# Optimization experiments

Measured on AMD Instinct MI355X. Metric: run time of the kernel, lower is better.

The kernel has to match this reference:

```python
import math
import jax, jax.numpy as jnp
import numpy as np

N = 50000          # nodes
E = 800000         # edges
IN_DIM = 128
HID = 128
OUT_DIM = 64
LAYER_NUM = 8      # -> LAYER_NUM - 2 = 6 GCN2Conv layers
NUM_CONVS = LAYER_NUM - 2
ALPHA = 0.1
THETA = 0.5
# PyG GCN2Conv: beta = log(theta / layer + 1); here every conv was built with layer = layer_num + 1
BETA = math.log(THETA / (LAYER_NUM + 1) + 1.0)


def setup_inputs() -> dict:
    key = jax.random.key(0)
    ks = jax.random.split(key, 10)
    x = jax.random.normal(ks[0], (N, IN_DIM), dtype=jnp.float32)
    edge_src = jax.random.randint(ks[1], (E,), 0, N, dtype=jnp.int32)
    edge_dst = jax.random.randint(ks[2], (E,), 0, N, dtype=jnp.int32)
    edge_weight = jax.random.uniform(ks[3], (E,), dtype=jnp.float32)
    s0 = 1.0 / math.sqrt(IN_DIM)
    s1 = 1.0 / math.sqrt(HID)
    W0 = jax.random.uniform(ks[4], (IN_DIM, HID), dtype=jnp.float32, minval=-s0, maxval=s0)
    b0 = jnp.zeros((HID,), dtype=jnp.float32)
    W1 = jax.random.uniform(ks[5], (HID, OUT_DIM), dtype=jnp.float32, minval=-s1, maxval=s1)
    b1 = jnp.zeros((OUT_DIM,), dtype=jnp.float32)
    conv_ws = jax.random.uniform(ks[6], (NUM_CONVS, HID, HID), dtype=jnp.float32, minval=-s1, maxval=s1)
    return {"x": x, "edge_src": edge_src, "edge_dst": edge_dst, "edge_weight": edge_weight,
            "W0": W0, "b0": b0, "W1": W1, "b1": b1, "conv_ws": conv_ws}


def reference(x, edge_src, edge_dst, edge_weight, W0, b0, W1, b1, conv_ws):
    # linear[0] + relu (dropout=0.0 -> identity)
    h = jnp.maximum(x @ W0 + b0, 0.0)          # [N, HID]
    x0 = h
    for i in range(NUM_CONVS):
        # weighted neighbor sum: out[i] = sum_{(j->i)} w_ji * h[j]
        msgs = h[edge_src] * edge_weight[:, None]               # [E, HID]
        agg = jax.ops.segment_sum(msgs, edge_dst, num_segments=N)
        # GCN2Conv (shared_weights=True): z = (1-alpha)*Ah + alpha*x0; out = (1-beta)*z + beta*(z W)
        z = agg * (1.0 - ALPHA) + ALPHA * x0
        h = z * (1.0 - BETA) + BETA * (z @ conv_ws[i])
        h = jnp.maximum(h, 0.0)
    return h @ W1 + b1                          # [N, OUT_DIM]
```

## Files before the change

kernel.cpp:

```cpp
#include <hip/hip_runtime.h>
#include <cstdint>
#include <cstddef>


#define NN 50000
#define EE 800000

constexpr float ALPHA   = 0.1f;
constexpr float BETA_C  = 0.05406722127027574f;

constexpr int NB = (NN + 255) / 256;
constexpr int HB = (EE + 255) / 256;
constexpr int PREP_TOT = 128 * 128 + 6 * 128 * 128 + 64 * 128;
constexpr int PB = (PREP_TOT + 255) / 256;
constexpr int SLICE = NN / 8;
constexpr int GA = (NN + 63) / 64;
constexpr int AGGB = 8 * ((GA + 1) / 2);

typedef unsigned short u16;
typedef unsigned int   u32;
typedef __attribute__((ext_vector_type(8))) short short8;
typedef __attribute__((ext_vector_type(4))) float f32x4;

__device__ __forceinline__ float bf2f(u16 u) {
    union { float f; u32 i; } c; c.i = ((u32)u) << 16; return c.f;
}
__device__ __forceinline__ u16 f2bf(float f) {
    union { float f; u32 i; } c; c.f = f;
    u32 r = c.i + 0x7fffu + ((c.i >> 16) & 1u);
    return (u16)(r >> 16);
}

__global__ void k_hist_prep(const int* __restrict__ edst, int* __restrict__ deg,
                            const float* __restrict__ W0, const float* __restrict__ cw,
                            const float* __restrict__ W1, u16* __restrict__ w0t,
                            u16* __restrict__ wft, u16* __restrict__ w1t, int E) {
    int b = blockIdx.x;
    if (b < HB) {
        int i = b * 256 + threadIdx.x;
        if (i < E) atomicAdd(&deg[edst[i]], 1);
    } else {
        int i = (b - HB) * 256 + threadIdx.x;
        if (i < 16384) {
            int n = i >> 7, k = i & 127;
            w0t[i] = f2bf(W0[k * 128 + n]);
        } else if (i < 16384 + 6 * 16384) {
            int r = i - 16384;
            int l = r >> 14; int t = r & 16383;
            int n = t >> 7, k = t & 127;
            float v = BETA_C * cw[l * 16384 + k * 128 + n]
                      + ((k == n) ? (1.f - BETA_C) : 0.f);
            wft[r] = f2bf(v);
        } else if (i < PREP_TOT) {
            int r = i - (16384 + 6 * 16384);
            int n = r >> 7, k = r & 127;
            w1t[r] = f2bf(W1[k * 64 + n]);
        }
    }
}

__global__ __launch_bounds__(256) void k_scan_lb(const int* __restrict__ deg,
                                                 int* __restrict__ bsum,
                                                 int* __restrict__ offs,
                                                 int* __restrict__ cur) {
    __shared__ int sh[256];
    __shared__ int sw[4];
    const int c = blockIdx.x, tid = threadIdx.x;
    const int i = c * 256 + tid;
    int v = (i < NN) ? deg[i] : 0;
    sh[tid] = v;
    __syncthreads();
#pragma unroll
    for (int o = 1; o < 256; o <<= 1) {
        int u = (tid >= o) ? sh[tid - o] : 0;
        __syncthreads();
        sh[tid] += u;
        __syncthreads();
    }
    if (tid == 255) atomicExch(&bsum[c], sh[255] + 1);
    int part = 0;
    for (int t = tid; t < c; t += 256) {
        int b;
        do { b = atomicAdd(&bsum[t], 0); } while (b == 0);
        part += b - 1;
    }
#pragma unroll
    for (int o = 32; o > 0; o >>= 1) part += __shfl_down(part, o);
    if ((tid & 63) == 0) sw[tid >> 6] = part;
    __syncthreads();
    const int base = sw[0] + sw[1] + sw[2] + sw[3];
    const int ex = base + sh[tid] - v;
    if (i < NN) {
        offs[i] = ex;
        cur[i]  = ex;
        if (i == NN - 1) offs[NN] = ex + v;
    }
}

__global__ void k_bucket_x(const int* __restrict__ src, const int* __restrict__ dst,
                           const float* __restrict__ w, int* __restrict__ cur,
                           u32* __restrict__ ep, int E) {
    const int slice = blockIdx.x & 7;
    const int i = (blockIdx.x >> 3) * 256 + threadIdx.x;
    if (i >= E) return;
    const int d = dst[i];
    const int lo = slice * SLICE;
    if (d >= lo && d < lo + SLICE) {
        int pos = atomicAdd(&cur[d], 1);
        ep[pos] = ((u32)f2bf(w[i]) << 16) | (u32)src[i];
    }
}

__global__ __launch_bounds__(256) void k_agg_z(const int* __restrict__ offs,
                                               const u32* __restrict__ ep,
                                               const u16* __restrict__ hs,
                                               const u16* __restrict__ x0s,
                                               u16* __restrict__ zs) {
    const int bid = blockIdx.x;
    const int s     = (bid & 7) >> 1;
    const int chunk = ((bid >> 3) << 1) | (bid & 1);
    const int lane = threadIdx.x & 63;
    const int wave = threadIdx.x >> 6;
    const int g  = lane >> 2;
    const int f4 = lane & 3;
    const int n  = chunk * 64 + wave * 16 + g;
    const int nc = n < NN ? n : NN - 1;
    const uint4* table = (const uint4*)(hs + (size_t)s * NN * 32);

    const int beg = offs[nc], end = offs[nc + 1];
    float a0 = 0.f, a1 = 0.f, a2 = 0.f, a3 = 0.f;
    float a4 = 0.f, a5 = 0.f, a6 = 0.f, a7 = 0.f;
    int e = beg;
    for (; e + 7 < end; e += 8) {
        u32 r[8]; uint4 v[8];
#pragma unroll
        for (int j = 0; j < 8; ++j) r[j] = ep[e + j];
#pragma unroll
        for (int j = 0; j < 8; ++j)
            v[j] = table[(size_t)(r[j] & 0xffffu) * 4 + f4];
#pragma unroll
        for (int j = 0; j < 8; ++j) {
            float w = bf2f((u16)(r[j] >> 16));
            a0 += w * bf2f((u16)v[j].x);  a1 += w * bf2f((u16)(v[j].x >> 16));
            a2 += w * bf2f((u16)v[j].y);  a3 += w * bf2f((u16)(v[j].y >> 16));
            a4 += w * bf2f((u16)v[j].z);  a5 += w * bf2f((u16)(v[j].z >> 16));
            a6 += w * bf2f((u16)v[j].w);  a7 += w * bf2f((u16)(v[j].w >> 16));
        }
    }
    for (; e < end; ++e) {
        u32 r = ep[e];
        uint4 v = table[(size_t)(r & 0xffffu) * 4 + f4];
        float w = bf2f((u16)(r >> 16));
        a0 += w * bf2f((u16)v.x);  a1 += w * bf2f((u16)(v.x >> 16));
        a2 += w * bf2f((u16)v.y);  a3 += w * bf2f((u16)(v.y >> 16));
        a4 += w * bf2f((u16)v.z);  a5 += w * bf2f((u16)(v.z >> 16));
        a6 += w * bf2f((u16)v.w);  a7 += w * bf2f((u16)(v.w >> 16));
    }
    if (n < NN) {
        const size_t idx = (size_t)s * NN * 4 + (size_t)n * 4 + f4;
        uint4 xv = ((const uint4*)x0s)[idx];
        float z0 = (1.f - ALPHA) * a0 + ALPHA * bf2f((u16)xv.x);
        float z1 = (1.f - ALPHA) * a1 + ALPHA * bf2f((u16)(xv.x >> 16));
        float z2 = (1.f - ALPHA) * a2 + ALPHA * bf2f((u16)xv.y);
        float z3 = (1.f - ALPHA) * a3 + ALPHA * bf2f((u16)(xv.y >> 16));
        float z4 = (1.f - ALPHA) * a4 + ALPHA * bf2f((u16)xv.z);
        float z5 = (1.f - ALPHA) * a5 + ALPHA * bf2f((u16)(xv.z >> 16));
        float z6 = (1.f - ALPHA) * a6 + ALPHA * bf2f((u16)xv.w);
        float z7 = (1.f - ALPHA) * a7 + ALPHA * bf2f((u16)(xv.w >> 16));
        uint4 o;
        o.x = (u32)f2bf(z0) | ((u32)f2bf(z1) << 16);
        o.y = (u32)f2bf(z2) | ((u32)f2bf(z3) << 16);
        o.z = (u32)f2bf(z4) | ((u32)f2bf(z5) << 16);
        o.w = (u32)f2bf(z6) | ((u32)f2bf(z7) << 16);
        ((uint4*)zs)[idx] = o;
    }
}

template <int MODE>
__global__ __launch_bounds__(256) void k_gemm_mfma(const void* __restrict__ Av,
                                                   const u16* __restrict__ Wt,
                                                   const float* __restrict__ bias,
                                                   void* __restrict__ Cv, int M) {
    const int lane = threadIdx.x & 63;
    const int wave = threadIdx.x >> 6;
    const int q = lane >> 4;
    const int m16 = lane & 15;
    const int node = blockIdx.x * 64 + wave * 16 + m16;
    const int nload = node < M ? node : M - 1;

    short8 zf[4];
    if (MODE == 0) {
        const float* xp = (const float*)Av + (size_t)nload * 128 + q * 8;
#pragma unroll
        for (int s = 0; s < 4; ++s) {
            float4 u0 = *(const float4*)(xp + s * 32);
            float4 u1 = *(const float4*)(xp + s * 32 + 4);
            short8 z;
            z[0] = (short)f2bf(u0.x); z[1] = (short)f2bf(u0.y);
            z[2] = (short)f2bf(u0.z); z[3] = (short)f2bf(u0.w);
            z[4] = (short)f2bf(u1.x); z[5] = (short)f2bf(u1.y);
            z[6] = (short)f2bf(u1.z); z[7] = (short)f2bf(u1.w);
            zf[s] = z;
        }
    } else {
        const u16* ap = (const u16*)Av;
#pragma unroll
        for (int s = 0; s < 4; ++s)
            zf[s] = *(const short8*)(ap + (size_t)s * NN * 32 + (size_t)nload * 32 + q * 8);
    }

    f32x4 acc[8];
#pragma unroll
    for (int c = 0; c < 8; ++c) {
        f32x4 a = {0.f, 0.f, 0.f, 0.f};
        const u16* wp = Wt + (size_t)(c * 16 + m16) * 128 + q * 8;
#pragma unroll
        for (int s = 0; s < 4; ++s) {
            short8 wf = *(const short8*)(wp + s * 32);
            a = __builtin_amdgcn_mfma_f32_16x16x32_bf16(wf, zf[s], a, 0, 0, 0);
        }
        acc[c] = a;
    }

    if (node < M) {
#pragma unroll
        for (int c = 0; c < 8; ++c) {
            const int f0 = c * 16 + q * 4;
            float v0 = acc[c][0], v1 = acc[c][1], v2 = acc[c][2], v3 = acc[c][3];
            if (MODE == 0) {
                float4 bv = *(const float4*)(bias + f0);
                v0 += bv.x; v1 += bv.y; v2 += bv.z; v3 += bv.w;
            }
            v0 = v0 > 0.f ? v0 : 0.f;
            v1 = v1 > 0.f ? v1 : 0.f;
            v2 = v2 > 0.f ? v2 : 0.f;
            v3 = v3 > 0.f ? v3 : 0.f;
            ushort4 o;
            o.x = f2bf(v0); o.y = f2bf(v1); o.z = f2bf(v2); o.w = f2bf(v3);
            *(ushort4*)((u16*)Cv + (size_t)(f0 >> 5) * NN * 32
                        + (size_t)node * 32 + (f0 & 31)) = o;
        }
    }
}

__global__ __launch_bounds__(256) void k_gemm_last(const u16* __restrict__ z,
                                                   const u16* __restrict__ wf5,
                                                   const u16* __restrict__ w1t,
                                                   const float* __restrict__ b1,
                                                   float* __restrict__ out) {
    __shared__ __align__(16) u16 hl[4][16][136];
    const int lane = threadIdx.x & 63;
    const int wave = threadIdx.x >> 6;
    const int q = lane >> 4;
    const int m16 = lane & 15;
    const int node = blockIdx.x * 64 + wave * 16 + m16;
    const int nload = node < NN ? node : NN - 1;

    short8 zf[4];
#pragma unroll
    for (int s = 0; s < 4; ++s)
        zf[s] = *(const short8*)(z + (size_t)s * NN * 32 + (size_t)nload * 32 + q * 8);

#pragma unroll
    for (int c = 0; c < 8; ++c) {
        f32x4 a = {0.f, 0.f, 0.f, 0.f};
        const u16* wp = wf5 + (size_t)(c * 16 + m16) * 128 + q * 8;
#pragma unroll
        for (int s = 0; s < 4; ++s) {
            short8 wf = *(const short8*)(wp + s * 32);
            a = __builtin_amdgcn_mfma_f32_16x16x32_bf16(wf, zf[s], a, 0, 0, 0);
        }
        float v0 = a[0] > 0.f ? a[0] : 0.f;
        float v1 = a[1] > 0.f ? a[1] : 0.f;
        float v2 = a[2] > 0.f ? a[2] : 0.f;
        float v3 = a[3] > 0.f ? a[3] : 0.f;
        ushort4 o;
        o.x = f2bf(v0); o.y = f2bf(v1); o.z = f2bf(v2); o.w = f2bf(v3);
        *(ushort4*)&hl[wave][m16][c * 16 + q * 4] = o;
    }
    __syncthreads();

    short8 hf[4];
#pragma unroll
    for (int s = 0; s < 4; ++s)
        hf[s] = *(const short8*)&hl[wave][m16][s * 32 + q * 8];

#pragma unroll
    for (int c = 0; c < 4; ++c) {
        f32x4 a = {0.f, 0.f, 0.f, 0.f};
        const u16* wp = w1t + (size_t)(c * 16 + m16) * 128 + q * 8;
#pragma unroll
        for (int s = 0; s < 4; ++s) {
            short8 wf = *(const short8*)(wp + s * 32);
            a = __builtin_amdgcn_mfma_f32_16x16x32_bf16(wf, hf[s], a, 0, 0, 0);
        }
        if (node < NN) {
            const int f0 = c * 16 + q * 4;
            float4 bv = *(const float4*)(b1 + f0);
            float4 o;
            o.x = a[0] + bv.x; o.y = a[1] + bv.y;
            o.z = a[2] + bv.z; o.w = a[3] + bv.w;
            *(float4*)(out + (size_t)node * 64 + f0) = o;
        }
    }
}


extern "C" void kernel_launch(void* const* d_in, const int* in_sizes, int n_in,
                              void* d_out, int out_size, void* d_ws, size_t ws_size,
                              hipStream_t stream) {
    const float* x    = (const float*)d_in[0];
    const int*   esrc = (const int*)d_in[1];
    const int*   edst = (const int*)d_in[2];
    const float* ew   = (const float*)d_in[3];
    const float* W0   = (const float*)d_in[4];
    const float* b0   = (const float*)d_in[5];
    const float* W1   = (const float*)d_in[6];
    const float* b1   = (const float*)d_in[7];
    const float* cw   = (const float*)d_in[8];
    float* out = (float*)d_out;

    const int N = NN, E = EE;

    u32*  ep4   = (u32*)d_ws;
    u16*  x0s   = (u16*)(ep4 + E);
    u16*  hb1   = x0s + (size_t)4 * N * 32;
    u16*  hb2   = hb1 + (size_t)4 * N * 32;
    u16*  zsb   = hb2 + (size_t)4 * N * 32;
    u16*  w0t   = zsb + (size_t)4 * N * 32;
    u16*  wft   = w0t + 128 * 128;
    u16*  w1t   = wft + 6 * 128 * 128;
    int*  deg   = (int*)(w1t + 64 * 128);
    int*  bsum  = deg  + N;
    int*  offs  = bsum + NB;
    int*  cur   = offs + N + 1;

    hipMemsetAsync(deg, 0, (size_t)(N + NB) * sizeof(int), stream);
    k_hist_prep<<<HB + PB, 256, 0, stream>>>(edst, deg, W0, cw, W1, w0t, wft, w1t, E);
    k_scan_lb<<<NB, 256, 0, stream>>>(deg, bsum, offs, cur);
    k_bucket_x<<<HB * 8, 256, 0, stream>>>(esrc, edst, ew, cur, ep4, E);

    k_gemm_mfma<0><<<GA, 256, 0, stream>>>(x, w0t, b0, x0s, N);

    const u16* hin = x0s;
    u16* houts[5] = {hb1, hb2, hb1, hb2, hb1};
    for (int i = 0; i < 5; ++i) {
        k_agg_z<<<AGGB, 256, 0, stream>>>(offs, ep4, hin, x0s, zsb);
        k_gemm_mfma<1><<<GA, 256, 0, stream>>>(zsb, wft + (size_t)i * 16384,
                                               nullptr, houts[i], N);
        hin = houts[i];
    }

    k_agg_z<<<AGGB, 256, 0, stream>>>(offs, ep4, hin, x0s, zsb);
    k_gemm_last<<<GA, 256, 0, stream>>>(zsb, wft + (size_t)5 * 16384, w1t, b1, out);
}
```

Measured before the change: 503.9 us.

## Process destination nodes in degree-sorted order and pack bf16 unpack into float2 FMAs

Adds a degree histogram and a counting sort that builds a node permutation grouped by in-degree. The aggregation kernel then walks nodes in that order, so the lanes of a wave handle nodes with similar edge counts and less loop divergence. The inner accumulation is also rewritten to use float2 vector multiply-adds with a cheaper bf16 unpack. The cost is one extra sort kernel, an indirect perm lookup, and scattered x0/z row accesses, since neighbouring lanes now touch non-contiguous rows.

```diff
diff --git a/kernel.cpp b/kernel.cpp
--- a/kernel.cpp
+++ b/kernel.cpp
@@ -16,11 +16,13 @@
 constexpr int SLICE = NN / 8;
 constexpr int GA = (NN + 63) / 64;
 constexpr int AGGB = 8 * ((GA + 1) / 2);
+constexpr int DBK = 128;
 
 typedef unsigned short u16;
 typedef unsigned int   u32;
 typedef __attribute__((ext_vector_type(8))) short short8;
 typedef __attribute__((ext_vector_type(4))) float f32x4;
+typedef __attribute__((ext_vector_type(2))) float f32x2;
 
 __device__ __forceinline__ float bf2f(u16 u) {
     union { float f; u32 i; } c; c.i = ((u32)u) << 16; return c.f;
@@ -29,6 +31,12 @@
     union { float f; u32 i; } c; c.f = f;
     u32 r = c.i + 0x7fffu + ((c.i >> 16) & 1u);
     return (u16)(r >> 16);
+}
+__device__ __forceinline__ f32x2 up2(u32 v) {
+    f32x2 r;
+    r.x = __uint_as_float(v << 16);
+    r.y = __uint_as_float(v & 0xffff0000u);
+    return r;
 }
 
 __global__ void k_hist_prep(const int* __restrict__ edst, int* __restrict__ deg,
@@ -62,14 +70,18 @@
 __global__ __launch_bounds__(256) void k_scan_lb(const int* __restrict__ deg,
                                                  int* __restrict__ bsum,
                                                  int* __restrict__ offs,
-                                                 int* __restrict__ cur) {
+                                                 int* __restrict__ cur,
+                                                 int* __restrict__ dhist) {
     __shared__ int sh[256];
     __shared__ int sw[4];
+    __shared__ int lhist[DBK];
     const int c = blockIdx.x, tid = threadIdx.x;
     const int i = c * 256 + tid;
+    if (tid < DBK) lhist[tid] = 0;
     int v = (i < NN) ? deg[i] : 0;
     sh[tid] = v;
     __syncthreads();
+    if (i < NN) atomicAdd(&lhist[v < DBK ? v : DBK - 1], 1);
 #pragma unroll
     for (int o = 1; o < 256; o <<= 1) {
         int u = (tid >= o) ? sh[tid - o] : 0;
@@ -95,6 +107,41 @@
         cur[i]  = ex;
         if (i == NN - 1) offs[NN] = ex + v;
     }
+    __syncthreads();
+    if (tid < DBK && lhist[tid] > 0) atomicAdd(&dhist[tid], lhist[tid]);
+}
+
+__global__ __launch_bounds__(256) void k_dsort(const int* __restrict__ deg,
+                                               const int* __restrict__ dhist,
+                                               int* __restrict__ dcur,
+                                               int* __restrict__ perm) {
+    __shared__ int db[DBK];
+    __shared__ int lh[DBK];
+    __shared__ int lb[DBK];
+    const int tid = threadIdx.x;
+    const int i = blockIdx.x * 256 + tid;
+    if (tid < DBK) { db[tid] = dhist[tid]; lh[tid] = 0; }
+    __syncthreads();
+#pragma unroll
+    for (int o = 1; o < DBK; o <<= 1) {
+        int u = (tid >= o && tid < DBK) ? db[tid - o] : 0;
+        __syncthreads();
+        if (tid < DBK) db[tid] += u;
+        __syncthreads();
+    }
+    if (tid < DBK) db[tid] -= dhist[tid];
+    __syncthreads();
+    int b = 0, lr = 0;
+    if (i < NN) {
+        int d = deg[i];
+        b = d < DBK ? d : DBK - 1;
+        lr = atomicAdd(&lh[b], 1);
+    }
+    __syncthreads();
+    if (tid < DBK && lh[tid] > 0)
+        lb[tid] = db[tid] + atomicAdd(&dcur[tid], lh[tid]);
+    __syncthreads();
+    if (i < NN) perm[lb[b] + lr] = i;
 }
 
 __global__ void k_bucket_x(const int* __restrict__ src, const int* __restrict__ dst,
@@ -115,7 +162,8 @@
                                                const u32* __restrict__ ep,
                                                const u16* __restrict__ hs,
                                                const u16* __restrict__ x0s,
-                                               u16* __restrict__ zs) {
+                                               u16* __restrict__ zs,
+                                               const int* __restrict__ perm) {
     const int bid = blockIdx.x;
     const int s     = (bid & 7) >> 1;
     const int chunk = ((bid >> 3) << 1) | (bid & 1);
@@ -124,12 +172,11 @@
     const int g  = lane >> 2;
     const int f4 = lane & 3;
     const int n  = chunk * 64 + wave * 16 + g;
-    const int nc = n < NN ? n : NN - 1;
+    const int pn = perm[n < NN ? n : NN - 1];
     const uint4* table = (const uint4*)(hs + (size_t)s * NN * 32);
 
-    const int beg = offs[nc], end = offs[nc + 1];
-    float a0 = 0.f, a1 = 0.f, a2 = 0.f, a3 = 0.f;
-    float a4 = 0.f, a5 = 0.f, a6 = 0.f, a7 = 0.f;
+    const int beg = offs[pn], end = offs[pn + 1];
+    f32x2 a01 = {0.f, 0.f}, a23 = {0.f, 0.f}, a45 = {0.f, 0.f}, a67 = {0.f, 0.f};
     int e = beg;
     for (; e + 7 < end; e += 8) {
         u32 r[8]; uint4 v[8];
@@ -140,33 +187,36 @@
             v[j] = table[(size_t)(r[j] & 0xffffu) * 4 + f4];
 #pragma unroll
         for (int j = 0; j < 8; ++j) {
-            float w = bf2f((u16)(r[j] >> 16));
-            a0 += w * bf2f((u16)v[j].x);  a1 += w * bf2f((u16)(v[j].x >> 16));
-            a2 += w * bf2f((u16)v[j].y);  a3 += w * bf2f((u16)(v[j].y >> 16));
-            a4 += w * bf2f((u16)v[j].z);  a5 += w * bf2f((u16)(v[j].z >> 16));
-            a6 += w * bf2f((u16)v[j].w);  a7 += w * bf2f((u16)(v[j].w >> 16));
+            float wv = __uint_as_float(r[j] & 0xffff0000u);
+            f32x2 w2 = {wv, wv};
+            a01 += up2(v[j].x) * w2;
+            a23 += up2(v[j].y) * w2;
+            a45 += up2(v[j].z) * w2;
+            a67 += up2(v[j].w) * w2;
         }
     }
     for (; e < end; ++e) {
         u32 r = ep[e];
         uint4 v = table[(size_t)(r & 0xffffu) * 4 + f4];
-        float w = bf2f((u16)(r >> 16));
-        a0 += w * bf2f((u16)v.x);  a1 += w * bf2f((u16)(v.x >> 16));
-        a2 += w * bf2f((u16)v.y);  a3 += w * bf2f((u16)(v.y >> 16));
-        a4 += w * bf2f((u16)v.z);  a5 += w * bf2f((u16)(v.z >> 16));
-        a6 += w * bf2f((u16)v.w);  a7 += w * bf2f((u16)(v.w >> 16));
+        float wv = __uint_as_float(r & 0xffff0000u);
+        f32x2 w2 = {wv, wv};
+        a01 += up2(v.x) * w2;
+        a23 += up2(v.y) * w2;
+        a45 += up2(v.z) * w2;
+        a67 += up2(v.w) * w2;
     }
     if (n < NN) {
-        const size_t idx = (size_t)s * NN * 4 + (size_t)n * 4 + f4;
+        const size_t idx = (size_t)s * NN * 4 + (size_t)pn * 4 + f4;
         uint4 xv = ((const uint4*)x0s)[idx];
-        float z0 = (1.f - ALPHA) * a0 + ALPHA * bf2f((u16)xv.x);
-        float z1 = (1.f - ALPHA) * a1 + ALPHA * bf2f((u16)(xv.x >> 16));
-        float z2 = (1.f - ALPHA) * a2 + ALPHA * bf2f((u16)xv.y);
-        float z3 = (1.f - ALPHA) * a3 + ALPHA * bf2f((u16)(xv.y >> 16));
-        float z4 = (1.f - ALPHA) * a4 + ALPHA * bf2f((u16)xv.z);
-        float z5 = (1.f - ALPHA) * a5 + ALPHA * bf2f((u16)(xv.z >> 16));
-        float z6 = (1.f - ALPHA) * a6 + ALPHA * bf2f((u16)xv.w);
-        float z7 = (1.f - ALPHA) * a7 + ALPHA * bf2f((u16)(xv.w >> 16));
+        f32x2 x01 = up2(xv.x), x23 = up2(xv.y), x45 = up2(xv.z), x67 = up2(xv.w);
+        float z0 = (1.f - ALPHA) * a01.x + ALPHA * x01.x;
+        float z1 = (1.f - ALPHA) * a01.y + ALPHA * x01.y;
+        float z2 = (1.f - ALPHA) * a23.x + ALPHA * x23.x;
+        float z3 = (1.f - ALPHA) * a23.y + ALPHA * x23.y;
+        float z4 = (1.f - ALPHA) * a45.x + ALPHA * x45.x;
+        float z5 = (1.f - ALPHA) * a45.y + ALPHA * x45.y;
+        float z6 = (1.f - ALPHA) * a67.x + ALPHA * x67.x;
+        float z7 = (1.f - ALPHA) * a67.y + ALPHA * x67.y;
         uint4 o;
         o.x = (u32)f2bf(z0) | ((u32)f2bf(z1) << 16);
         o.y = (u32)f2bf(z2) | ((u32)f2bf(z3) << 16);
@@ -320,37 +370,39 @@
     const float* cw   = (const float*)d_in[8];
     float* out = (float*)d_out;
 
-    const int N = NN, E = EE;
-
-    u32*  ep4   = (u32*)d_ws;
-    u16*  x0s   = (u16*)(ep4 + E);
-    u16*  hb1   = x0s + (size_t)4 * N * 32;
-    u16*  hb2   = hb1 + (size_t)4 * N * 32;
-    u16*  zsb   = hb2 + (size_t)4 * N * 32;
-    u16*  w0t   = zsb + (size_t)4 * N * 32;
-    u16*  wft   = w0t + 128 * 128;
-    u16*  w1t   = wft + 6 * 128 * 128;
-    int*  deg   = (int*)(w1t + 64 * 128);
-    int*  bsum  = deg  + N;
-    int*  offs  = bsum + NB;
-    int*  cur   = offs + N + 1;
-
-    hipMemsetAsync(deg, 0, (size_t)(N + NB) * sizeof(int), stream);
-    k_hist_prep<<<HB + PB, 256, 0, stream>>>(edst, deg, W0, cw, W1, w0t, wft, w1t, E);
-    k_scan_lb<<<NB, 256, 0, stream>>>(deg, bsum, offs, cur);
-    k_bucket_x<<<HB * 8, 256, 0, stream>>>(esrc, edst, ew, cur, ep4, E);
-
-    k_gemm_mfma<0><<<GA, 256, 0, stream>>>(x, w0t, b0, x0s, N);
+    u32* ep4 = (u32*)d_ws;
+    u16* x0s = (u16*)(ep4 + EE);
+    u16* hb1 = x0s + (size_t)4 * NN * 32;
+    u16* hb2 = hb1 + (size_t)4 * NN * 32;
+    u16* zsb = hb2 + (size_t)4 * NN * 32;
+    u16* w0t = zsb + (size_t)4 * NN * 32;
+    u16* wft = w0t + 128 * 128;
+    u16* w1t = wft + 6 * 128 * 128;
+    int* deg = (int*)(w1t + 64 * 128);
+    int* bsum = deg + NN;
+    int* dhist = bsum + NB;
+    int* dcur = dhist + DBK;
+    int* offs = dcur + DBK;
+    int* cur = offs + NN + 1;
+    int* perm = cur + NN;
+
+    (void)hipMemsetAsync(deg, 0, (size_t)(NN + NB + 2 * DBK) * sizeof(int), stream);
+    k_hist_prep<<<HB + PB, 256, 0, stream>>>(edst, deg, W0, cw, W1, w0t, wft, w1t, EE);
+    k_scan_lb<<<NB, 256, 0, stream>>>(deg, bsum, offs, cur, dhist);
+    k_dsort<<<NB, 256, 0, stream>>>(deg, dhist, dcur, perm);
+    k_bucket_x<<<HB * 8, 256, 0, stream>>>(esrc, edst, ew, cur, ep4, EE);
+
+    k_gemm_mfma<0><<<GA, 256, 0, stream>>>(x, w0t, b0, x0s, NN);
 
     const u16* hin = x0s;
     u16* houts[5] = {hb1, hb2, hb1, hb2, hb1};
     for (int i = 0; i < 5; ++i) {
-        k_agg_z<<<AGGB, 256, 0, stream>>>(offs, ep4, hin, x0s, zsb);
+        k_agg_z<<<AGGB, 256, 0, stream>>>(offs, ep4, hin, x0s, zsb, perm);
         k_gemm_mfma<1><<<GA, 256, 0, stream>>>(zsb, wft + (size_t)i * 16384,
-                                               nullptr, houts[i], N);
+                                               nullptr, houts[i], NN);
         hin = houts[i];
     }
 
-    k_agg_z<<<AGGB, 256, 0, stream>>>(offs, ep4, hin, x0s, zsb);
+    k_agg_z<<<AGGB, 256, 0, stream>>>(offs, ep4, hin, x0s, zsb, perm);
     k_gemm_last<<<GA, 256, 0, stream>>>(zsb, wft + (size_t)5 * 16384, w1t, b1, out);
 }
```

Result: slower. 519.5 us (+3.1%).
